# Kernel tuning notes

Hardware: AMD Instinct MI355X
Metric: run time of the kernel (lower is better)

The kernel has to match this reference:

```python
import jax, jax.numpy as jnp
import numpy as np

K = 16
RADIUS = 1.0
N = 16384
SEQ = 8


def _knn(pc, k):
    """Brute-force kNN of pc against itself. pc: (1, n, 3).
    Returns (dist, idx) each (1, n, k), sorted ascending by distance,
    matching pointutils.knn semantics (Euclidean distance)."""
    x2 = jnp.sum(pc * pc, axis=-1)  # (1, n)
    # d2[b,i,j] = ||p_i - p_j||^2 via expansion; avoids (n,n,3) intermediate
    d2 = x2[:, :, None] + x2[:, None, :] - 2.0 * jnp.einsum('bnd,bmd->bnm', pc, pc)
    d2 = jnp.maximum(d2, 0.0)
    neg_d2, idx = jax.lax.top_k(-d2, k)  # k smallest distances
    dist = jnp.sqrt(jnp.maximum(-neg_d2, 0.0))
    return dist, idx


def setup_inputs() -> dict:
    key = jax.random.key(0)
    k1, k2, k3 = jax.random.split(key, 3)
    return {
        'pc_source': jax.random.normal(k1, (1, N, 3), dtype=jnp.float32),
        'pred_flow': jax.random.normal(k2, (SEQ, N, 3), dtype=jnp.float32),
        'weights': jax.random.uniform(k3, (N,), dtype=jnp.float32),
    }


def reference(pc_source, pred_flow, weights):
    # flow: (seq, 3, n)
    flow = jnp.transpose(pred_flow, (0, 2, 1))
    dist, idx = _knn(pc_source, K)  # (1, n, k)
    # replace out-of-radius neighbors with the nearest (self) index
    idx = jnp.where(dist > RADIUS, idx[:, :, 0:1], idx)
    idx = idx[0]  # (n, k); identical for all sequence steps
    # grouping_operation: gather neighbor flows -> (seq, 3, n, k)
    nn_flow = flow[:, :, idx]
    diff = flow[:, :, :, None] - nn_flow  # (seq, 3, n, k)
    # L2 norm over channel dim (loss_norm=2), safe at 0 (self-neighbor)
    sq = jnp.sum(diff * diff, axis=1)  # (seq, n, k)
    norm = jnp.where(sq > 0, jnp.sqrt(jnp.where(sq > 0, sq, 1.0)), 0.0)
    loss = norm.mean(axis=-1)  # (seq, n)
    loss = loss * weights[None, :]
    loss = loss.sum(axis=1)  # (seq,)
    wsum = weights.sum()
    loss = jnp.where(wsum > 0, loss / wsum, loss)
    return loss.mean()
```

## Files before the change

### kernel.cpp

```cpp
#include <hip/hip_runtime.h>
#include <math.h>

#define NPTS  16384
#define KNN   16
#define SEQV  8
#define NW    16
#define BATCH 8
#define CAPM  15
#define CAPR  1.001f
#define NBKT  256
#define BSCALE 56.8888f
#define HBLK  16
#define NGRP  256

#define SLOT(arr, t, col) arr[(t) * 1024 + (col)]

#define WS_HIST   256
#define WS_STARTS 16640
#define WS_SIDX   17920
#define WS_SORTED 83488
#define WS_FLOWT  345760

__device__ __forceinline__ unsigned umin_(unsigned a, unsigned b) { return a < b ? a : b; }
__device__ __forceinline__ unsigned umax_(unsigned a, unsigned b) { return a > b ? a : b; }

__device__ __forceinline__ int nbucket(float x) { return (int)fminf(x * BSCALE, 255.0f); }

__device__ __forceinline__ void merge_one(unsigned keys[KNN], unsigned kk) {
    if (kk < keys[KNN - 1]) {
#pragma unroll
        for (int u = 0; u < KNN; ++u) {
            unsigned lo = umin_(kk, keys[u]);
            kk = umax_(kk, keys[u]);
            keys[u] = lo;
        }
    }
}

__device__ __forceinline__ void merge16(unsigned k[KNN], const unsigned o[KNN]) {
    unsigned v[KNN];
#pragma unroll
    for (int i = 0; i < KNN; ++i) v[i] = umin_(k[i], o[KNN - 1 - i]);
#pragma unroll
    for (int d = 8; d >= 1; d >>= 1) {
#pragma unroll
        for (int i = 0; i < KNN; ++i) {
            if ((i & d) == 0) {
                unsigned lo = umin_(v[i], v[i + d]);
                unsigned hi = umax_(v[i], v[i + d]);
                v[i] = lo; v[i + d] = hi;
            }
        }
    }
#pragma unroll
    for (int i = 0; i < KNN; ++i) k[i] = v[i];
}

__device__ __forceinline__ void tree_load_merge(unsigned* uS, unsigned keys[KNN], int src) {
    unsigned o[KNN];
#pragma unroll
    for (int t = 0; t < KNN; ++t) o[t] = SLOT(uS, t, src);
    merge16(keys, o);
}

__global__ __launch_bounds__(1024) void hist_kernel(
    const float* __restrict__ pc, const float* __restrict__ flow,
    unsigned* __restrict__ hist, float4* __restrict__ flowT)
{
    __shared__ unsigned h[NBKT];
    const int tid = threadIdx.x;
    if (tid < NBKT) h[tid] = 0u;
    __syncthreads();
    const int i = blockIdx.x * 1024 + tid;
    const float x = pc[3 * i + 0], y = pc[3 * i + 1], z = pc[3 * i + 2];
    const float n = sqrtf(fmaf(x, x, fmaf(y, y, z * z)));
    atomicAdd(&h[nbucket(n)], 1u);
#pragma unroll
    for (int s = 0; s < SEQV; ++s) {
        const float* fp = flow + (size_t)s * NPTS * 3 + 3 * i;
        flowT[s * NPTS + i] = make_float4(fp[0], fp[1], fp[2], 0.0f);
    }
    __syncthreads();
    if (tid < NBKT) hist[tid * HBLK + blockIdx.x] = h[tid];
}

__global__ __launch_bounds__(1024) void scatter_kernel(
    const float* __restrict__ pc, const unsigned* __restrict__ hist,
    unsigned* __restrict__ starts, float* __restrict__ accum,
    unsigned* __restrict__ sidx, float4* __restrict__ sorted4)
{
    __shared__ unsigned sH[NBKT];
    __shared__ unsigned sBase[NBKT];
    __shared__ unsigned sCnt[NBKT];
    const int tid = threadIdx.x;
    const int b   = blockIdx.x;

    unsigned own = 0, pre = 0;
    if (tid < NBKT) {
        const unsigned* row = hist + tid * HBLK;
        unsigned s = 0, p = 0;
#pragma unroll
        for (int k = 0; k < HBLK; ++k) {
            const unsigned c = row[k];
            if (k < b) p += c;
            s += c;
        }
        own = s; pre = p;
        sH[tid] = s;
        sCnt[tid] = 0u;
    }
    __syncthreads();
    for (int off = 1; off < NBKT; off <<= 1) {
        unsigned a = 0u;
        if (tid < NBKT && tid >= off) a = sH[tid - off];
        __syncthreads();
        if (tid < NBKT) sH[tid] += a;
        __syncthreads();
    }
    if (tid < NBKT) {
        const unsigned excl = sH[tid] - own;
        sBase[tid] = excl + pre;
        if (b == 0) starts[tid] = excl;
    }
    if (b == 0 && tid == 0) starts[NBKT] = NPTS;
    if (b == 0 && tid < 8) ((unsigned*)accum)[tid] = 0u;
    __syncthreads();

    const int i = b * 1024 + tid;
    const float x = pc[3 * i + 0], y = pc[3 * i + 1], z = pc[3 * i + 2];
    const float c2 = fmaf(x, x, fmaf(y, y, z * z));
    const int bin = nbucket(sqrtf(c2));
    const unsigned rank = atomicAdd(&sCnt[bin], 1u);
    const unsigned pos = sBase[bin] + rank;
    sorted4[pos] = make_float4(-2.0f * x, -2.0f * y, -2.0f * z, c2);
    sidx[pos] = (unsigned)i;
    if (b == 0 && tid < 8) {
        sorted4[NPTS + tid] = make_float4(0.0f, 0.0f, 0.0f, 1e18f);
        sidx[NPTS + tid] = 0u;
    }
}

__global__ __launch_bounds__(1024, 4) void mega_kernel(
    const float4* __restrict__ sorted, const unsigned* __restrict__ sidx,
    const unsigned* __restrict__ starts, const float4* __restrict__ flowT,
    const float* __restrict__ wts, float* __restrict__ accum,
    float* __restrict__ out)
{
    __shared__ unsigned uS[1024 * 16];
    float* sred = (float*)&uS[15 * 1024 + 1000];
    float* sTau = (float*)&uS[16320];

    const int tid  = threadIdx.x;
    const int lane = tid & 63;
    const int wv   = __builtin_amdgcn_readfirstlane(tid >> 6);
    const int is   = blockIdx.x * 64 + lane;

    const float4 mi = sorted[is];
    const float qx = -0.5f * mi.x;
    const float qy = -0.5f * mi.y;
    const float qz = -0.5f * mi.z;
    const float q2 = mi.w;
    const unsigned iorig = sidx[is];
    const float analytic = 0.19072f * exp2f(0.480898f * q2);
    const float tau0 = fminf(analytic, CAPR);

    const float nq = sqrtf(q2);
    float nmin = nq, nmax = nq;
#pragma unroll
    for (int off = 32; off > 0; off >>= 1) {
        nmin = fminf(nmin, __shfl_xor(nmin, off));
        nmax = fmaxf(nmax, __shfl_xor(nmax, off));
    }
    const float r0 = sqrtf(fminf(0.19072f * exp2f(0.480898f * nmax * nmax), CAPR));
    const int blo = nbucket(fmaxf(nmin - r0, 0.0f));
    const int bhi = nbucket(nmax + r0);
    const int kT0 = __builtin_amdgcn_readfirstlane((int)starts[blo]) >> 3;
    const int kTe = (__builtin_amdgcn_readfirstlane((int)starts[bhi + 1]) + 7) >> 3;

    unsigned keys[KNN];
#pragma unroll
    for (int t = 0; t < KNN; ++t) keys[t] = 0xFFFFFFFFu;
    int cnt = 0;
    unsigned* buf = &uS[tid * CAPM];

    {
        float taufs = tau0 - q2;
        float4 A[BATCH], Bv[BATCH];
        unsigned As[BATCH], Bs[BATCH];

        auto proc = [&](const float4* C, const unsigned* S) {
#pragma unroll
            for (int q = 0; q < BATCH; ++q) {
                const float4 c = C[q];
                float d2p = fmaf(c.x, qx, fmaf(c.y, qy, fmaf(c.z, qz, c.w)));
                bool acc = d2p <= taufs;
                if (__any(acc)) {
                    if (acc) {
                        float d2 = fmaxf(d2p + q2, 0.0f);
                        buf[cnt] = (__float_as_uint(d2) & 0xFFFFC000u) | S[q];
                        ++cnt;
                    }
                    if (__any(cnt >= CAPM - 1)) {
#pragma unroll 1
                        for (int t = 0; t < CAPM - 1; ++t)
                            merge_one(keys, (t < cnt) ? buf[t] : 0xFFFFFFFFu);
                        cnt = 0;
                        float d16n = __uint_as_float(keys[KNN - 1] & 0xFFFFC000u);
                        taufs = fminf(taufs, fmaf(d16n, 1.0002f, 1e-6f) - q2);
                    }
                }
            }
        };

        int k = kT0 + wv;
        bool hA = (k < kTe);
        if (hA) { const float4* bp = sorted + (k << 3); const unsigned* sp = sidx + (k << 3);
#pragma unroll
            for (int q = 0; q < BATCH; ++q) { A[q] = bp[q]; As[q] = sp[q]; } }
        while (hA) {
            int k2 = k + 64; bool hB = (k2 < kTe);
            if (hB) { const float4* bp = sorted + (k2 << 3); const unsigned* sp = sidx + (k2 << 3);
#pragma unroll
                for (int q = 0; q < BATCH; ++q) { Bv[q] = bp[q]; Bs[q] = sp[q]; } }
            proc(A, As);
            if (!hB) break;
            int k3 = k2 + 64; bool hC = (k3 < kTe);
            if (hC) { const float4* bp = sorted + (k3 << 3); const unsigned* sp = sidx + (k3 << 3);
#pragma unroll
                for (int q = 0; q < BATCH; ++q) { A[q] = bp[q]; As[q] = sp[q]; } }
            proc(Bv, Bs);
            k = k3; hA = hC;
        }
#pragma unroll 1
        for (int t = 0; t < CAPM - 1; ++t)
            merge_one(keys, (t < cnt) ? buf[t] : 0xFFFFFFFFu);
        cnt = 0;
    }

    unsigned keys2[KNN];
#pragma unroll
    for (int t = 0; t < KNN; ++t) keys2[t] = keys[t];

    __syncthreads();

#pragma unroll
    for (int t = 0; t < KNN; ++t) SLOT(uS, t, tid) = keys[t];
    __syncthreads();
    if (wv < 8) {
        tree_load_merge(uS, keys, tid + 512);
#pragma unroll
        for (int t = 0; t < KNN; ++t) SLOT(uS, t, tid) = keys[t];
    }
    __syncthreads();
    if (wv < 4) {
        tree_load_merge(uS, keys, tid + 256);
#pragma unroll
        for (int t = 0; t < KNN; ++t) SLOT(uS, t, tid) = keys[t];
    }
    __syncthreads();
    if (wv < 2) {
        tree_load_merge(uS, keys, tid + 128);
#pragma unroll
        for (int t = 0; t < KNN; ++t) SLOT(uS, t, tid) = keys[t];
    }
    __syncthreads();
    if (wv == 0) {
        tree_load_merge(uS, keys, tid + 64);
        const float d16 = __uint_as_float(keys[KNN - 1] & 0xFFFFC000u);
        const float tf  = fmaf(d16, 1.0002f, 1e-6f);
        const bool fail = !(tf <= tau0);
        const float tv = fail ? CAPR : tf;
        sTau[lane] = tv;
        float tm = tv;
#pragma unroll
        for (int off = 32; off > 0; off >>= 1) tm = fmaxf(tm, __shfl_xor(tm, off));
        unsigned long long bw = __ballot(fail && (analytic < CAPR));
        if (lane == 0) { uS[16316] = (bw != 0ull) ? 1u : 0u; ((float*)uS)[16317] = tm; }
    }
    __syncthreads();

    float taufs = sTau[lane] - q2;
    const unsigned anyWide = __builtin_amdgcn_readfirstlane(uS[16316]);
    const float rA = sqrtf(((float*)uS)[16317]);
    int kA0, kAe;
    if (anyWide) { kA0 = 0; kAe = NPTS / 8; }
    else {
        int bloA = nbucket(fmaxf(nmin - rA, 0.0f));
        int bhiA = nbucket(nmax + rA);
        kA0 = __builtin_amdgcn_readfirstlane((int)starts[bloA]) >> 3;
        kAe = (__builtin_amdgcn_readfirstlane((int)starts[bhiA + 1]) + 7) >> 3;
    }
#pragma unroll
    for (int t = 0; t < KNN; ++t) keys[t] = keys2[t];
    {
        float4 A[BATCH], Bv[BATCH];
        unsigned As[BATCH], Bs[BATCH];

        auto proc = [&](const float4* C, const unsigned* S) {
#pragma unroll
            for (int q = 0; q < BATCH; ++q) {
                const float4 c = C[q];
                float d2p = fmaf(c.x, qx, fmaf(c.y, qy, fmaf(c.z, qz, c.w)));
                bool acc = d2p <= taufs;
                if (__any(acc)) {
                    if (acc) {
                        float d2 = fmaxf(d2p + q2, 0.0f);
                        buf[cnt] = (__float_as_uint(d2) & 0xFFFFC000u) | S[q];
                        ++cnt;
                    }
                    if (__any(cnt >= CAPM - 1)) {
#pragma unroll 1
                        for (int t = 0; t < CAPM - 1; ++t)
                            merge_one(keys, (t < cnt) ? buf[t] : 0xFFFFFFFFu);
                        cnt = 0;
                        float d16n = __uint_as_float(keys[KNN - 1] & 0xFFFFC000u);
                        taufs = fminf(taufs, fmaf(d16n, 1.0002f, 1e-6f) - q2);
                    }
                }
            }
        };

        auto skipb = [&](int k) -> bool {
            return (!anyWide) && (k < kTe) && (((k - kT0 - wv) & 63) == 0);
        };
        int k = kA0 + ((wv - (kA0 - kT0)) & 15);
        if (skipb(k)) k += 16;
        bool hA = (k < kAe);
        if (hA) { const float4* bp = sorted + (k << 3); const unsigned* sp = sidx + (k << 3);
#pragma unroll
            for (int q = 0; q < BATCH; ++q) { A[q] = bp[q]; As[q] = sp[q]; } }
        while (hA) {
            int k2 = k + 16; if (skipb(k2)) k2 += 16;
            bool hB = (k2 < kAe);
            if (hB) { const float4* bp = sorted + (k2 << 3); const unsigned* sp = sidx + (k2 << 3);
#pragma unroll
                for (int q = 0; q < BATCH; ++q) { Bv[q] = bp[q]; Bs[q] = sp[q]; } }
            proc(A, As);
            if (!hB) break;
            int k3 = k2 + 16; if (skipb(k3)) k3 += 16;
            bool hC = (k3 < kAe);
            if (hC) { const float4* bp = sorted + (k3 << 3); const unsigned* sp = sidx + (k3 << 3);
#pragma unroll
                for (int q = 0; q < BATCH; ++q) { A[q] = bp[q]; As[q] = sp[q]; } }
            proc(Bv, Bs);
            k = k3; hA = hC;
        }
#pragma unroll 1
        for (int t = 0; t < CAPM - 1; ++t)
            merge_one(keys, (t < cnt) ? buf[t] : 0xFFFFFFFFu);
    }
    __syncthreads();

#pragma unroll
    for (int t = 0; t < KNN; ++t) SLOT(uS, t, tid) = keys[t];
    __syncthreads();
    if (wv < 8) {
        tree_load_merge(uS, keys, tid + 512);
#pragma unroll
        for (int t = 0; t < KNN; ++t) SLOT(uS, t, tid) = keys[t];
    }
    __syncthreads();
    if (wv < 4) {
        tree_load_merge(uS, keys, tid + 256);
#pragma unroll
        for (int t = 0; t < KNN; ++t) SLOT(uS, t, tid) = keys[t];
    }
    __syncthreads();
    if (wv < 2) {
        tree_load_merge(uS, keys, tid + 128);
#pragma unroll
        for (int t = 0; t < KNN; ++t) SLOT(uS, t, tid) = keys[t];
    }
    __syncthreads();
    if (wv == 0) {
        tree_load_merge(uS, keys, tid + 64);
        const int id0 = (int)(keys[0] & 0x3FFFu);
#pragma unroll
        for (int t = 0; t < KNN; ++t) {
            float d2t = __uint_as_float(keys[t] & 0xFFFFC000u);
            int   j   = (int)(keys[t] & 0x3FFFu);
            SLOT(uS, t, lane) = (unsigned)((d2t > 1.0f) ? id0 : j);
        }
    }
    __syncthreads();

    {
        const int s  = wv & 7;
        const int kh = wv >> 3;
        const float4* fs4 = flowT + (size_t)s * NPTS;
        const float4 qf = fs4[iorig];

        float sum = 0.0f;
#pragma unroll
        for (int z = 0; z < 8; ++z) {
            int j = (int)SLOT(uS, kh * 8 + z, lane);
            const float4 v = fs4[j];
            float dx = qf.x - v.x;
            float dy = qf.y - v.y;
            float dz = qf.z - v.z;
            float sq = fmaf(dx, dx, fmaf(dy, dy, dz * dz));
            sum += (sq > 0.0f) ? sqrtf(sq) : 0.0f;
        }

        float contrib = wts[iorig] * sum;
#pragma unroll
        for (int off = 32; off > 0; off >>= 1) contrib += __shfl_down(contrib, off);
        if (lane == 0) sred[wv] = contrib;

        if (wv == 0) {
            float wi = wts[iorig];
#pragma unroll
            for (int off = 32; off > 0; off >>= 1) wi += __shfl_down(wi, off);
            if (lane == 0) atomicAdd(&accum[1], wi);
        }
        __syncthreads();

        if (tid == 0) {
            float c = 0.0f;
#pragma unroll
            for (int t = 0; t < NW; ++t) c += sred[t];
            atomicAdd(&accum[0], c);
            __threadfence();
            unsigned ticket = atomicAdd((unsigned*)accum + 2, 1u);
            if (ticket == gridDim.x - 1) {
                float a  = atomicAdd(&accum[0], 0.0f);
                float ws = atomicAdd(&accum[1], 0.0f);
                float v  = a / (float)(KNN * SEQV);
                out[0] = (ws > 0.0f) ? (v / ws) : v;
            }
        }
    }
}

extern "C" void kernel_launch(void* const* d_in, const int* in_sizes, int n_in,
                              void* d_out, int out_size, void* d_ws, size_t ws_size,
                              hipStream_t stream)
{
    const float* pc   = (const float*)d_in[0];
    const float* flow = (const float*)d_in[1];
    const float* wts  = (const float*)d_in[2];
    float* out = (float*)d_out;

    float*    accum  = (float*)d_ws;
    unsigned* hist   = (unsigned*)((char*)d_ws + WS_HIST);
    unsigned* starts = (unsigned*)((char*)d_ws + WS_STARTS);
    unsigned* sidx   = (unsigned*)((char*)d_ws + WS_SIDX);
    float4*   sorted = (float4*)  ((char*)d_ws + WS_SORTED);
    float4*   flowT  = (float4*)  ((char*)d_ws + WS_FLOWT);

    hist_kernel   <<<HBLK, 1024, 0, stream>>>(pc, flow, hist, flowT);
    scatter_kernel<<<HBLK, 1024, 0, stream>>>(pc, hist, starts, accum, sidx, sorted);
    mega_kernel   <<<NGRP, 1024, 0, stream>>>(sorted, sidx, starts, flowT, wts, accum, out);
}
```

Baseline: 133.7 us.

## Scan candidate tiles outward from center with adaptive radius shrink

The candidate scan in the kNN kernel changes from strided forward passes to bidirectional sweeps starting at the middle of the bucket range. Odd waves walk downward and even waves upward, and every fourth iteration each wave recomputes a wave-max radius from its current threshold to tighten its scan bound. The analytic initial radius constant is lowered, and the preprocessing kernels use 64 blocks of 256 threads instead of 16 blocks of 1024. These changes aim to cut the number of candidate tiles scanned and to improve parallelism in preprocessing, at the cost of extra shuffles and global loads of bucket starts, plus a smaller initial radius that may trigger more wide fallbacks.

After: 144.1 us. +7.8%, slower.

```diff
diff --git a/kernel.cpp b/kernel.cpp
--- a/kernel.cpp
+++ b/kernel.cpp
@@ -10,16 +10,16 @@
 #define CAPR  1.001f
 #define NBKT  256
 #define BSCALE 56.8888f
-#define HBLK  16
+#define HBLK  64
 #define NGRP  256
 
 #define SLOT(arr, t, col) arr[(t) * 1024 + (col)]
 
 #define WS_HIST   256
-#define WS_STARTS 16640
-#define WS_SIDX   17920
-#define WS_SORTED 83488
-#define WS_FLOWT  345760
+#define WS_STARTS 65792
+#define WS_SIDX   67072
+#define WS_SORTED 132640
+#define WS_FLOWT  394912
 
 __device__ __forceinline__ unsigned umin_(unsigned a, unsigned b) { return a < b ? a : b; }
 __device__ __forceinline__ unsigned umax_(unsigned a, unsigned b) { return a > b ? a : b; }
@@ -63,15 +63,15 @@
     merge16(keys, o);
 }
 
-__global__ __launch_bounds__(1024) void hist_kernel(
+__global__ __launch_bounds__(256) void hist_kernel(
     const float* __restrict__ pc, const float* __restrict__ flow,
     unsigned* __restrict__ hist, float4* __restrict__ flowT)
 {
     __shared__ unsigned h[NBKT];
     const int tid = threadIdx.x;
-    if (tid < NBKT) h[tid] = 0u;
-    __syncthreads();
-    const int i = blockIdx.x * 1024 + tid;
+    h[tid] = 0u;
+    __syncthreads();
+    const int i = blockIdx.x * 256 + tid;
     const float x = pc[3 * i + 0], y = pc[3 * i + 1], z = pc[3 * i + 2];
     const float n = sqrtf(fmaf(x, x, fmaf(y, y, z * z)));
     atomicAdd(&h[nbucket(n)], 1u);
@@ -81,10 +81,10 @@
         flowT[s * NPTS + i] = make_float4(fp[0], fp[1], fp[2], 0.0f);
     }
     __syncthreads();
-    if (tid < NBKT) hist[tid * HBLK + blockIdx.x] = h[tid];
-}
-
-__global__ __launch_bounds__(1024) void scatter_kernel(
+    hist[tid * HBLK + blockIdx.x] = h[tid];
+}
+
+__global__ __launch_bounds__(256) void scatter_kernel(
     const float* __restrict__ pc, const unsigned* __restrict__ hist,
     unsigned* __restrict__ starts, float* __restrict__ accum,
     unsigned* __restrict__ sidx, float4* __restrict__ sorted4)
@@ -96,10 +96,10 @@
     const int b   = blockIdx.x;
 
     unsigned own = 0, pre = 0;
-    if (tid < NBKT) {
+    {
         const unsigned* row = hist + tid * HBLK;
         unsigned s = 0, p = 0;
-#pragma unroll
+#pragma unroll 8
         for (int k = 0; k < HBLK; ++k) {
             const unsigned c = row[k];
             if (k < b) p += c;
@@ -112,12 +112,12 @@
     __syncthreads();
     for (int off = 1; off < NBKT; off <<= 1) {
         unsigned a = 0u;
-        if (tid < NBKT && tid >= off) a = sH[tid - off];
+        if (tid >= off) a = sH[tid - off];
         __syncthreads();
-        if (tid < NBKT) sH[tid] += a;
+        sH[tid] += a;
         __syncthreads();
     }
-    if (tid < NBKT) {
+    {
         const unsigned excl = sH[tid] - own;
         sBase[tid] = excl + pre;
         if (b == 0) starts[tid] = excl;
@@ -126,7 +126,7 @@
     if (b == 0 && tid < 8) ((unsigned*)accum)[tid] = 0u;
     __syncthreads();
 
-    const int i = b * 1024 + tid;
+    const int i = b * 256 + tid;
     const float x = pc[3 * i + 0], y = pc[3 * i + 1], z = pc[3 * i + 2];
     const float c2 = fmaf(x, x, fmaf(y, y, z * z));
     const int bin = nbucket(sqrtf(c2));
@@ -161,7 +161,7 @@
     const float qz = -0.5f * mi.z;
     const float q2 = mi.w;
     const unsigned iorig = sidx[is];
-    const float analytic = 0.19072f * exp2f(0.480898f * q2);
+    const float analytic = 0.14304f * exp2f(0.480898f * q2);
     const float tau0 = fminf(analytic, CAPR);
 
     const float nq = sqrtf(q2);
@@ -171,7 +171,7 @@
         nmin = fminf(nmin, __shfl_xor(nmin, off));
         nmax = fmaxf(nmax, __shfl_xor(nmax, off));
     }
-    const float r0 = sqrtf(fminf(0.19072f * exp2f(0.480898f * nmax * nmax), CAPR));
+    const float r0 = sqrtf(fminf(0.14304f * exp2f(0.480898f * nmax * nmax), CAPR));
     const int blo = nbucket(fmaxf(nmin - r0, 0.0f));
     const int bhi = nbucket(nmax + r0);
     const int kT0 = __builtin_amdgcn_readfirstlane((int)starts[blo]) >> 3;
@@ -320,25 +320,49 @@
             }
         };
 
+        const int dir = (wv & 1) ? -8 : 8;
+        const int c0  = kA0 + ((kAe - kA0) >> 1);
+        int kLo = kA0, kHi = kAe;
         auto skipb = [&](int k) -> bool {
-            return (!anyWide) && (k < kTe) && (((k - kT0 - wv) & 63) == 0);
+            return (!anyWide) && (k >= kT0) && (k < kTe)
+                && (((k - kT0) & 63) < 16);
         };
-        int k = kA0 + ((wv - (kA0 - kT0)) & 15);
-        if (skipb(k)) k += 16;
-        bool hA = (k < kAe);
+        auto advk = [&](int k) { do { k += dir; } while (skipb(k)); return k; };
+        auto inb  = [&](int k) { return (dir > 0) ? (k < kHi) : (k >= kLo); };
+
+        int k = (dir > 0) ? (c0 + (wv >> 1)) : (c0 - 1 - (wv >> 1));
+        while (skipb(k)) k += dir;
+        int iter = 0;
+        bool hA = inb(k);
         if (hA) { const float4* bp = sorted + (k << 3); const unsigned* sp = sidx + (k << 3);
 #pragma unroll
             for (int q = 0; q < BATCH; ++q) { A[q] = bp[q]; As[q] = sp[q]; } }
         while (hA) {
-            int k2 = k + 16; if (skipb(k2)) k2 += 16;
-            bool hB = (k2 < kAe);
+            int k2 = advk(k);
+            if (((++iter) & 3) == 0) {
+                float td = taufs + q2;
+#pragma unroll
+                for (int off = 32; off > 0; off >>= 1)
+                    td = fmaxf(td, __shfl_xor(td, off));
+                float rr = sqrtf(td);
+                if (dir > 0) {
+                    int bh = nbucket(nmax + rr);
+                    int ne = (__builtin_amdgcn_readfirstlane((int)starts[bh + 1]) + 7) >> 3;
+                    kHi = (ne < kHi) ? ne : kHi;
+                } else {
+                    int bl = nbucket(fmaxf(nmin - rr, 0.0f));
+                    int ns = __builtin_amdgcn_readfirstlane((int)starts[bl]) >> 3;
+                    kLo = (ns > kLo) ? ns : kLo;
+                }
+            }
+            bool hB = inb(k2);
             if (hB) { const float4* bp = sorted + (k2 << 3); const unsigned* sp = sidx + (k2 << 3);
 #pragma unroll
                 for (int q = 0; q < BATCH; ++q) { Bv[q] = bp[q]; Bs[q] = sp[q]; } }
             proc(A, As);
             if (!hB) break;
-            int k3 = k2 + 16; if (skipb(k3)) k3 += 16;
-            bool hC = (k3 < kAe);
+            int k3 = advk(k2);
+            bool hC = inb(k3);
             if (hC) { const float4* bp = sorted + (k3 << 3); const unsigned* sp = sidx + (k3 << 3);
 #pragma unroll
                 for (int q = 0; q < BATCH; ++q) { A[q] = bp[q]; As[q] = sp[q]; } }
@@ -448,7 +472,7 @@
     float4*   sorted = (float4*)  ((char*)d_ws + WS_SORTED);
     float4*   flowT  = (float4*)  ((char*)d_ws + WS_FLOWT);
 
-    hist_kernel   <<<HBLK, 1024, 0, stream>>>(pc, flow, hist, flowT);
-    scatter_kernel<<<HBLK, 1024, 0, stream>>>(pc, hist, starts, accum, sidx, sorted);
+    hist_kernel   <<<HBLK, 256, 0, stream>>>(pc, flow, hist, flowT);
+    scatter_kernel<<<HBLK, 256, 0, stream>>>(pc, hist, starts, accum, sidx, sorted);
     mega_kernel   <<<NGRP, 1024, 0, stream>>>(sorted, sidx, starts, flowT, wts, accum, out);
 }
```
